# Kernel tuning notes

Measured on AMD Instinct MI355X. Metric: run time of the kernel, lower is better.

Reference implementation:

```python
import jax, jax.numpy as jnp
import numpy as np

N_NODES = 100000
N_EDGES = 1600000
D_FEAT = 64


def setup_inputs() -> dict:
    key = jax.random.key(0)
    k1, k2 = jax.random.split(key)
    x = jax.random.normal(k1, (N_NODES, D_FEAT), dtype=jnp.float32)
    edge_index = jax.random.randint(k2, (2, N_EDGES), 0, N_NODES, dtype=jnp.int64)
    return {"x": x, "edge_index": edge_index}


def reference(x, edge_index):
    # flow='source_to_target': j = edge_index[0] (source), i = edge_index[1] (target)
    # message: x_j = gather source node features along dim 0
    msgs = x[edge_index[0]]                      # [E, D]
    # aggregate: scatter-add messages to target nodes, dim_size = N
    out = jax.ops.segment_sum(msgs, edge_index[1], num_segments=x.shape[0])  # [N, D]
    # update: identity
    return out
```

## Files before the change

### kernel.cpp

```cpp
#include <hip/hip_runtime.h>

#define D_FEAT 64
#define SUBN 128
#define SUBN_SHIFT 7
#define NBINS_MAX 1024
#define SCAN_BLOCK 256
#define SCAN_ELEMS 1024
#define SCAN_SHIFT 10

__global__ __launch_bounds__(256) void k_atomic_scatter(
    const float* __restrict__ x, const int* __restrict__ src,
    const int* __restrict__ tgt, float* __restrict__ out, int n_edges)
{
    const int lane = threadIdx.x & 63;
    const int wave = threadIdx.x >> 6;
    const int e = blockIdx.x * 4 + wave;
    if (e >= n_edges) return;
    const float v = x[(long long)src[e] * D_FEAT + lane];
    atomicAdd(&out[(long long)tgt[e] * D_FEAT + lane], v);
}

__global__ __launch_bounds__(256) void k_convert_count(
    const float* __restrict__ x, unsigned short* __restrict__ xb, int n4,
    const int* __restrict__ tgt, int* __restrict__ cnt, int E, int NBINS, int CH)
{
    __shared__ int c[NBINS_MAX];
    const int tid = threadIdx.x;
    const int stride = gridDim.x * 256;
    for (int i = blockIdx.x * 256 + tid; i < n4; i += stride) {
        float4 f = ((const float4*)x)[i];
        ushort4 u;
        unsigned int b;
        b = __float_as_uint(f.x); u.x = (unsigned short)((b + 0x7fffu + ((b >> 16) & 1u)) >> 16);
        b = __float_as_uint(f.y); u.y = (unsigned short)((b + 0x7fffu + ((b >> 16) & 1u)) >> 16);
        b = __float_as_uint(f.z); u.z = (unsigned short)((b + 0x7fffu + ((b >> 16) & 1u)) >> 16);
        b = __float_as_uint(f.w); u.w = (unsigned short)((b + 0x7fffu + ((b >> 16) & 1u)) >> 16);
        ((ushort4*)xb)[i] = u;
    }
    for (int i = tid; i < NBINS; i += 256) c[i] = 0;
    __syncthreads();
    const int base = blockIdx.x * CH;
    const int lim = min(E, base + CH);
    for (int e = base + tid; e < lim; e += 256)
        atomicAdd(&c[tgt[e] >> SUBN_SHIFT], 1);
    __syncthreads();
    for (int i = tid; i < NBINS; i += 256) cnt[(size_t)blockIdx.x * NBINS + i] = c[i];
}

__global__ __launch_bounds__(SCAN_BLOCK) void k_scan_partial_T(
    const int* __restrict__ cnt, int* __restrict__ off,
    int* __restrict__ bsum, int M, int NBINS, int NBLK)
{
    __shared__ int lds[SCAN_BLOCK];
    const int tid = threadIdx.x;
    const int base = blockIdx.x * SCAN_ELEMS + tid * 4;
    int v[4];
#pragma unroll
    for (int k = 0; k < 4; ++k) {
        int i = base + k;
        if (i < M) {
            int bin = i / NBLK;
            int blk = i - bin * NBLK;
            v[k] = cnt[(size_t)blk * NBINS + bin];
        } else v[k] = 0;
    }
    const int tsum = v[0] + v[1] + v[2] + v[3];
    int val = tsum;
    lds[tid] = val;
    __syncthreads();
    for (int d = 1; d < SCAN_BLOCK; d <<= 1) {
        int add = (tid >= d) ? lds[tid - d] : 0;
        __syncthreads();
        val += add;
        lds[tid] = val;
        __syncthreads();
    }
    if (tid == SCAN_BLOCK - 1) bsum[blockIdx.x] = val;
    int p = val - tsum;
#pragma unroll
    for (int k = 0; k < 4; ++k) {
        int i = base + k;
        if (i < M) { off[i] = p; p += v[k]; }
    }
}

__global__ __launch_bounds__(1024) void k_scan_sums(int* __restrict__ bsum, int nb)
{
    __shared__ int lds[1024];
    const int tid = threadIdx.x;
    const int v = (tid < nb) ? bsum[tid] : 0;
    int val = v;
    lds[tid] = val;
    __syncthreads();
    for (int d = 1; d < 1024; d <<= 1) {
        int add = (tid >= d) ? lds[tid - d] : 0;
        __syncthreads();
        val += add;
        lds[tid] = val;
        __syncthreads();
    }
    if (tid < nb) bsum[tid] = val - v;
}

__global__ __launch_bounds__(256) void k_bin_scatter(
    const int* __restrict__ src, const int* __restrict__ tgt,
    const int* __restrict__ off, const int* __restrict__ bsum,
    int* __restrict__ binned, int E, int NBINS, int NBLK, int CH)
{
    __shared__ int ofs[NBINS_MAX];
    const int tid = threadIdx.x;
    const int b = blockIdx.x;
    for (int i = tid; i < NBINS; i += 256) {
        size_t idx = (size_t)i * NBLK + b;
        ofs[i] = off[idx] + bsum[idx >> SCAN_SHIFT];
    }
    __syncthreads();
    const int base = b * CH;
    const int lim = min(E, base + CH);
    for (int e = base + tid; e < lim; e += 256) {
        int t = tgt[e];
        int s = src[e];
        int bin = t >> SUBN_SHIFT;
        int p = atomicAdd(&ofs[bin], 1);
        binned[p] = (s << SUBN_SHIFT) | (t & (SUBN - 1));
    }
}

__global__ __launch_bounds__(256) void k_bin_sort(
    const int* __restrict__ binned, const int* __restrict__ off,
    const int* __restrict__ bsum,
    int* __restrict__ srcSorted, int* __restrict__ nodeOff,
    int E, int N, int NBLK, int NBINS)
{
    __shared__ int hist[SUBN];
    __shared__ int ofs[SUBN];
    const int tid = threadIdx.x;
    const int bin = blockIdx.x;
    const size_t i0 = (size_t)bin * NBLK;
    const int binStart = off[i0] + bsum[i0 >> SCAN_SHIFT];
    int binEnd;
    if (bin + 1 < NBINS) {
        const size_t i1 = (size_t)(bin + 1) * NBLK;
        binEnd = off[i1] + bsum[i1 >> SCAN_SHIFT];
    } else binEnd = E;
    if (tid < SUBN) hist[tid] = 0;
    __syncthreads();
    for (int e = binStart + tid; e < binEnd; e += 256)
        atomicAdd(&hist[binned[e] & (SUBN - 1)], 1);
    __syncthreads();
    int orig = (tid < SUBN) ? hist[tid] : 0;
    int val = orig;
    if (tid < SUBN) ofs[tid] = val;
    __syncthreads();
    for (int d = 1; d < SUBN; d <<= 1) {
        int add = (tid >= d && tid < SUBN) ? ofs[tid - d] : 0;
        __syncthreads();
        if (tid < SUBN) { val += add; ofs[tid] = val; }
        __syncthreads();
    }
    if (tid < SUBN) {
        int abs0 = binStart + (val - orig);
        ofs[tid] = abs0;
        int node = bin * SUBN + tid;
        if (node < N) nodeOff[node] = abs0;
    }
    if (bin == 0 && tid == 0) nodeOff[N] = E;
    __syncthreads();
    for (int e = binStart + tid; e < binEnd; e += 256) {
        int entry = binned[e];
        int p = atomicAdd(&ofs[entry & (SUBN - 1)], 1);
        srcSorted[p] = entry >> SUBN_SHIFT;
    }
}

__global__ __launch_bounds__(256) void k_gather_bf2(
    const unsigned short* __restrict__ xb, const int* __restrict__ srcSorted,
    const int* __restrict__ nodeOff, float* __restrict__ out, int N)
{
    const int lane = threadIdx.x & 63;
    const int wave = threadIdx.x >> 6;
    const int half = lane >> 5;
    const int hl = lane & 31;
    const int wid0 = blockIdx.x * 4 + wave;
    const int wstride = gridDim.x * 4;

    for (int v = wid0; v < N; v += wstride) {
        const int start = __builtin_amdgcn_readfirstlane(nodeOff[v]);
        const int end   = __builtin_amdgcn_readfirstlane(nodeOff[v + 1]);
        float acc0 = 0.f, acc1 = 0.f;
        int k = start;
        for (; k + 16 <= end; k += 16) {
            int s[8]; unsigned int u[8];
#pragma unroll
            for (int j = 0; j < 8; ++j) s[j] = srcSorted[k + 2 * j + half];
#pragma unroll
            for (int j = 0; j < 8; ++j)
                u[j] = *(const unsigned int*)(xb + (size_t)s[j] * D_FEAT + 2 * hl);
#pragma unroll
            for (int j = 0; j < 8; ++j) {
                acc0 += __uint_as_float(u[j] << 16);
                acc1 += __uint_as_float(u[j] & 0xffff0000u);
            }
        }
        if (k + 8 <= end) {
            int s[4]; unsigned int u[4];
#pragma unroll
            for (int j = 0; j < 4; ++j) s[j] = srcSorted[k + 2 * j + half];
#pragma unroll
            for (int j = 0; j < 4; ++j)
                u[j] = *(const unsigned int*)(xb + (size_t)s[j] * D_FEAT + 2 * hl);
#pragma unroll
            for (int j = 0; j < 4; ++j) {
                acc0 += __uint_as_float(u[j] << 16);
                acc1 += __uint_as_float(u[j] & 0xffff0000u);
            }
            k += 8;
        }
        if (k + 4 <= end) {
            int s[2]; unsigned int u[2];
#pragma unroll
            for (int j = 0; j < 2; ++j) s[j] = srcSorted[k + 2 * j + half];
#pragma unroll
            for (int j = 0; j < 2; ++j)
                u[j] = *(const unsigned int*)(xb + (size_t)s[j] * D_FEAT + 2 * hl);
#pragma unroll
            for (int j = 0; j < 2; ++j) {
                acc0 += __uint_as_float(u[j] << 16);
                acc1 += __uint_as_float(u[j] & 0xffff0000u);
            }
            k += 4;
        }
        for (; k < end; k += 2) {
            int e = k + half;
            unsigned int u = 0;
            if (e < end)
                u = *(const unsigned int*)(xb + (size_t)srcSorted[e] * D_FEAT + 2 * hl);
            acc0 += __uint_as_float(u << 16);
            acc1 += __uint_as_float(u & 0xffff0000u);
        }
        acc0 += __shfl_xor(acc0, 32, 64);
        acc1 += __shfl_xor(acc1, 32, 64);
        if (half == 0)
            *(float2*)(out + (size_t)v * D_FEAT + 2 * hl) = make_float2(acc0, acc1);
    }
}

__global__ __launch_bounds__(256) void k_gather(
    const float* __restrict__ x, const int* __restrict__ srcSorted,
    const int* __restrict__ nodeOff, float* __restrict__ out, int N)
{
    const int lane = threadIdx.x & 63;
    const int wave = threadIdx.x >> 6;
    const int v = blockIdx.x * 4 + wave;
    if (v >= N) return;
    const int start = __builtin_amdgcn_readfirstlane(nodeOff[v]);
    const int end   = __builtin_amdgcn_readfirstlane(nodeOff[v + 1]);
    float acc = 0.f;
    int k = start;
    for (; k + 16 <= end; k += 16) {
        int s[16];
#pragma unroll
        for (int j = 0; j < 16; ++j) s[j] = srcSorted[k + j];
        float a[16];
#pragma unroll
        for (int j = 0; j < 16; ++j) a[j] = x[(size_t)s[j] * D_FEAT + lane];
        float t0 = (a[0]+a[1])+(a[2]+a[3]), t1 = (a[4]+a[5])+(a[6]+a[7]);
        float t2 = (a[8]+a[9])+(a[10]+a[11]), t3 = (a[12]+a[13])+(a[14]+a[15]);
        acc += (t0 + t1) + (t2 + t3);
    }
    for (; k < end; ++k)
        acc += x[(size_t)srcSorted[k] * D_FEAT + lane];
    out[(size_t)v * D_FEAT + lane] = acc;
}

static inline size_t xbf_pad(int N) {
    return ((size_t)N * D_FEAT * 2 + 255) & ~(size_t)255;
}
static inline size_t ws_need(long long M, int E, int N, int with_bf) {
    size_t b = ((size_t)2 * M + 1024 + 2 * (size_t)E + N + 1) * sizeof(int);
    if (with_bf) b += xbf_pad(N);
    return b;
}

extern "C" void kernel_launch(void* const* d_in, const int* in_sizes, int n_in,
                              void* d_out, int out_size, void* d_ws, size_t ws_size,
                              hipStream_t stream)
{
    const float* x  = (const float*)d_in[0];
    const int*   ei = (const int*)d_in[1];
    const int E = in_sizes[1] / 2;
    const int N = out_size / D_FEAT;
    const int* src = ei;
    const int* tgt = ei + E;
    float* out = (float*)d_out;

    const int NBINS = (N + SUBN - 1) / SUBN;

    int CH = 0, NBLK = 0, USE_BF = 0; long long M = 0; int nScan = 0;
    const int ch_opts[4] = {2048, 4096, 8192, 16384};
    for (int bf = 1; bf >= 0 && CH == 0; --bf) {
        for (int c = 0; c < 4; ++c) {
            int ch = ch_opts[c];
            int nblk = (E + ch - 1) / ch;
            long long m = (long long)nblk * NBINS;
            int ns = (int)((m + SCAN_ELEMS - 1) / SCAN_ELEMS);
            if (ns <= 1024 && ws_need(m, E, N, bf) <= ws_size) {
                CH = ch; NBLK = nblk; M = m; nScan = ns; USE_BF = bf; break;
            }
        }
    }

    if (CH == 0 || NBINS > NBINS_MAX || (long long)N * SUBN >= (1LL << 31)) {
        hipMemsetAsync(d_out, 0, (size_t)out_size * sizeof(float), stream);
        k_atomic_scatter<<<(E + 3) / 4, 256, 0, stream>>>(x, src, tgt, out, E);
        return;
    }

    unsigned short* xbf = (unsigned short*)d_ws;
    int* cnt = (int*)((char*)d_ws + (USE_BF ? xbf_pad(N) : 0));
    int* off = cnt + M;
    int* bsum = off + M;
    int* binned = bsum + 1024;
    int* srcSorted = binned + E;
    int* nodeOff = srcSorted + E;

    const int n4 = USE_BF ? (N * D_FEAT / 4) : 0;
    k_convert_count<<<NBLK, 256, 0, stream>>>(x, xbf, n4, tgt, cnt, E, NBINS, CH);
    k_scan_partial_T<<<nScan, SCAN_BLOCK, 0, stream>>>(cnt, off, bsum, (int)M, NBINS, NBLK);
    k_scan_sums<<<1, 1024, 0, stream>>>(bsum, nScan);
    k_bin_scatter<<<NBLK, 256, 0, stream>>>(src, tgt, off, bsum, binned, E, NBINS, NBLK, CH);
    k_bin_sort<<<NBINS, 256, 0, stream>>>(binned, off, bsum, srcSorted, nodeOff, E, N, NBLK, NBINS);
    if (USE_BF)
        k_gather_bf2<<<2048, 256, 0, stream>>>(xbf, srcSorted, nodeOff, out, N);
    else
        k_gather<<<(N + 3) / 4, 256, 0, stream>>>(x, srcSorted, nodeOff, out, N);
}
```

Measured before the change: 97.91 us.

## Replace two-level transposed scan with atomic bin totals and cursor reservation

```diff
diff --git a/kernel.cpp b/kernel.cpp
--- a/kernel.cpp
+++ b/kernel.cpp
@@ -4,9 +4,6 @@
 #define SUBN 128
 #define SUBN_SHIFT 7
 #define NBINS_MAX 1024
-#define SCAN_BLOCK 256
-#define SCAN_ELEMS 1024
-#define SCAN_SHIFT 10
 
 __global__ __launch_bounds__(256) void k_atomic_scatter(
     const float* __restrict__ x, const int* __restrict__ src,
@@ -22,7 +19,8 @@
 
 __global__ __launch_bounds__(256) void k_convert_count(
     const float* __restrict__ x, unsigned short* __restrict__ xb, int n4,
-    const int* __restrict__ tgt, int* __restrict__ cnt, int E, int NBINS, int CH)
+    const int* __restrict__ tgt, int* __restrict__ cnt, int* __restrict__ binTotal,
+    int E, int NBINS, int CH)
 {
     __shared__ int c[NBINS_MAX];
     const int tid = threadIdx.x;
@@ -44,51 +42,20 @@
     for (int e = base + tid; e < lim; e += 256)
         atomicAdd(&c[tgt[e] >> SUBN_SHIFT], 1);
     __syncthreads();
-    for (int i = tid; i < NBINS; i += 256) cnt[(size_t)blockIdx.x * NBINS + i] = c[i];
-}
-
-__global__ __launch_bounds__(SCAN_BLOCK) void k_scan_partial_T(
-    const int* __restrict__ cnt, int* __restrict__ off,
-    int* __restrict__ bsum, int M, int NBINS, int NBLK)
-{
-    __shared__ int lds[SCAN_BLOCK];
-    const int tid = threadIdx.x;
-    const int base = blockIdx.x * SCAN_ELEMS + tid * 4;
-    int v[4];
-#pragma unroll
-    for (int k = 0; k < 4; ++k) {
-        int i = base + k;
-        if (i < M) {
-            int bin = i / NBLK;
-            int blk = i - bin * NBLK;
-            v[k] = cnt[(size_t)blk * NBINS + bin];
-        } else v[k] = 0;
-    }
-    const int tsum = v[0] + v[1] + v[2] + v[3];
-    int val = tsum;
-    lds[tid] = val;
-    __syncthreads();
-    for (int d = 1; d < SCAN_BLOCK; d <<= 1) {
-        int add = (tid >= d) ? lds[tid - d] : 0;
-        __syncthreads();
-        val += add;
-        lds[tid] = val;
-        __syncthreads();
-    }
-    if (tid == SCAN_BLOCK - 1) bsum[blockIdx.x] = val;
-    int p = val - tsum;
-#pragma unroll
-    for (int k = 0; k < 4; ++k) {
-        int i = base + k;
-        if (i < M) { off[i] = p; p += v[k]; }
-    }
-}
-
-__global__ __launch_bounds__(1024) void k_scan_sums(int* __restrict__ bsum, int nb)
+    for (int i = tid; i < NBINS; i += 256) {
+        int ci = c[i];
+        cnt[(size_t)blockIdx.x * NBINS + i] = ci;
+        if (ci) atomicAdd(&binTotal[i], ci);
+    }
+}
+
+__global__ __launch_bounds__(1024) void k_scan_bins(
+    const int* __restrict__ binTotal, int* __restrict__ binOff,
+    int* __restrict__ cursor, int NBINS, int E)
 {
     __shared__ int lds[1024];
     const int tid = threadIdx.x;
-    const int v = (tid < nb) ? bsum[tid] : 0;
+    const int v = (tid < NBINS) ? binTotal[tid] : 0;
     int val = v;
     lds[tid] = val;
     __syncthreads();
@@ -99,20 +66,25 @@
         lds[tid] = val;
         __syncthreads();
     }
-    if (tid < nb) bsum[tid] = val - v;
+    if (tid < NBINS) {
+        int ex = val - v;
+        binOff[tid] = ex;
+        cursor[tid] = ex;
+    }
+    if (tid == 0) binOff[NBINS] = E;
 }
 
 __global__ __launch_bounds__(256) void k_bin_scatter(
     const int* __restrict__ src, const int* __restrict__ tgt,
-    const int* __restrict__ off, const int* __restrict__ bsum,
-    int* __restrict__ binned, int E, int NBINS, int NBLK, int CH)
+    const int* __restrict__ cnt, int* __restrict__ cursor,
+    int* __restrict__ binned, int E, int NBINS, int CH)
 {
     __shared__ int ofs[NBINS_MAX];
     const int tid = threadIdx.x;
     const int b = blockIdx.x;
     for (int i = tid; i < NBINS; i += 256) {
-        size_t idx = (size_t)i * NBLK + b;
-        ofs[i] = off[idx] + bsum[idx >> SCAN_SHIFT];
+        int ci = cnt[(size_t)b * NBINS + i];
+        ofs[i] = ci ? atomicAdd(&cursor[i], ci) : 0;
     }
     __syncthreads();
     const int base = b * CH;
@@ -127,22 +99,16 @@
 }
 
 __global__ __launch_bounds__(256) void k_bin_sort(
-    const int* __restrict__ binned, const int* __restrict__ off,
-    const int* __restrict__ bsum,
+    const int* __restrict__ binned, const int* __restrict__ binOff,
     int* __restrict__ srcSorted, int* __restrict__ nodeOff,
-    int E, int N, int NBLK, int NBINS)
+    int E, int N, int NBINS)
 {
     __shared__ int hist[SUBN];
     __shared__ int ofs[SUBN];
     const int tid = threadIdx.x;
     const int bin = blockIdx.x;
-    const size_t i0 = (size_t)bin * NBLK;
-    const int binStart = off[i0] + bsum[i0 >> SCAN_SHIFT];
-    int binEnd;
-    if (bin + 1 < NBINS) {
-        const size_t i1 = (size_t)(bin + 1) * NBLK;
-        binEnd = off[i1] + bsum[i1 >> SCAN_SHIFT];
-    } else binEnd = E;
+    const int binStart = binOff[bin];
+    const int binEnd   = binOff[bin + 1];
     if (tid < SUBN) hist[tid] = 0;
     __syncthreads();
     for (int e = binStart + tid; e < binEnd; e += 256)
@@ -276,8 +242,14 @@
 static inline size_t xbf_pad(int N) {
     return ((size_t)N * D_FEAT * 2 + 255) & ~(size_t)255;
 }
-static inline size_t ws_need(long long M, int E, int N, int with_bf) {
-    size_t b = ((size_t)2 * M + 1024 + 2 * (size_t)E + N + 1) * sizeof(int);
+static inline size_t ws_need(int NBLK, int NBINS, int E, int N, int with_bf) {
+    size_t ints = (size_t)NBLK * NBINS
+                + NBINS
+                + (NBINS + 1)
+                + NBINS
+                + 2 * (size_t)E
+                + (N + 1);
+    size_t b = ints * sizeof(int);
     if (with_bf) b += xbf_pad(N);
     return b;
 }
@@ -296,16 +268,14 @@
 
     const int NBINS = (N + SUBN - 1) / SUBN;
 
-    int CH = 0, NBLK = 0, USE_BF = 0; long long M = 0; int nScan = 0;
-    const int ch_opts[4] = {2048, 4096, 8192, 16384};
+    int CH = 0, NBLK = 0, USE_BF = 0;
+    const int ch_opts[3] = {4096, 8192, 16384};
     for (int bf = 1; bf >= 0 && CH == 0; --bf) {
-        for (int c = 0; c < 4; ++c) {
+        for (int c = 0; c < 3; ++c) {
             int ch = ch_opts[c];
             int nblk = (E + ch - 1) / ch;
-            long long m = (long long)nblk * NBINS;
-            int ns = (int)((m + SCAN_ELEMS - 1) / SCAN_ELEMS);
-            if (ns <= 1024 && ws_need(m, E, N, bf) <= ws_size) {
-                CH = ch; NBLK = nblk; M = m; nScan = ns; USE_BF = bf; break;
+            if (ws_need(nblk, NBINS, E, N, bf) <= ws_size) {
+                CH = ch; NBLK = nblk; USE_BF = bf; break;
             }
         }
     }
@@ -318,18 +288,19 @@
 
     unsigned short* xbf = (unsigned short*)d_ws;
     int* cnt = (int*)((char*)d_ws + (USE_BF ? xbf_pad(N) : 0));
-    int* off = cnt + M;
-    int* bsum = off + M;
-    int* binned = bsum + 1024;
+    int* binTotal = cnt + (size_t)NBLK * NBINS;
+    int* binOff = binTotal + NBINS;
+    int* cursor = binOff + (NBINS + 1);
+    int* binned = cursor + NBINS;
     int* srcSorted = binned + E;
     int* nodeOff = srcSorted + E;
 
+    hipMemsetAsync(binTotal, 0, (size_t)NBINS * sizeof(int), stream);
     const int n4 = USE_BF ? (N * D_FEAT / 4) : 0;
-    k_convert_count<<<NBLK, 256, 0, stream>>>(x, xbf, n4, tgt, cnt, E, NBINS, CH);
-    k_scan_partial_T<<<nScan, SCAN_BLOCK, 0, stream>>>(cnt, off, bsum, (int)M, NBINS, NBLK);
-    k_scan_sums<<<1, 1024, 0, stream>>>(bsum, nScan);
-    k_bin_scatter<<<NBLK, 256, 0, stream>>>(src, tgt, off, bsum, binned, E, NBINS, NBLK, CH);
-    k_bin_sort<<<NBINS, 256, 0, stream>>>(binned, off, bsum, srcSorted, nodeOff, E, N, NBLK, NBINS);
+    k_convert_count<<<NBLK, 256, 0, stream>>>(x, xbf, n4, tgt, cnt, binTotal, E, NBINS, CH);
+    k_scan_bins<<<1, 1024, 0, stream>>>(binTotal, binOff, cursor, NBINS, E);
+    k_bin_scatter<<<NBLK, 256, 0, stream>>>(src, tgt, cnt, cursor, binned, E, NBINS, CH);
+    k_bin_sort<<<NBINS, 256, 0, stream>>>(binned, binOff, srcSorted, nodeOff, E, N, NBINS);
     if (USE_BF)
         k_gather_bf2<<<2048, 256, 0, stream>>>(xbf, srcSorted, nodeOff, out, N);
     else
```

Measured after the change: 115.9 us. 18.4% more time.
